# Performance work log

Hardware: AMD Instinct MI355X
Metric: run time of the kernel (lower is better)

The kernel has to match this reference:

```python
import jax, jax.numpy as jnp
import numpy as np

EPS = 1e-5  # torch BatchNorm1d default eps


def _bn(x, g, b, m, v):
    # x: [B, C, L]; params: [C] (inference-mode BN using running stats)
    scale = g / jnp.sqrt(v + EPS)
    return x * scale[None, :, None] + (b - m * scale)[None, :, None]


def setup_inputs() -> dict:
    key = jax.random.key(0)
    ks = jax.random.split(key, 16)
    B, C, L, I = 32, 256, 4096, 64
    d = {
        "x_a": jax.random.normal(ks[0], (B, C, L), jnp.float32),
        "x_b": jax.random.normal(ks[1], (B, C, L), jnp.float32),
        "x_c": jax.random.normal(ks[2], (B, C, L), jnp.float32),
        "w1": jax.random.normal(ks[3], (4, I, C), jnp.float32) * 0.05,
        "b1": jax.random.normal(ks[4], (4, I), jnp.float32) * 0.05,
        "bn1_g": jax.random.uniform(ks[5], (4, I), jnp.float32, 0.5, 1.5),
        "bn1_b": jax.random.normal(ks[6], (4, I), jnp.float32) * 0.05,
        "bn1_m": jax.random.normal(ks[7], (4, I), jnp.float32) * 0.05,
        "bn1_v": jax.random.uniform(ks[8], (4, I), jnp.float32, 0.5, 1.5),
        "w2": jax.random.normal(ks[9], (4, C, I), jnp.float32) * 0.05,
        "b2": jax.random.normal(ks[10], (4, C), jnp.float32) * 0.05,
        "bn2_g": jax.random.uniform(ks[11], (4, C), jnp.float32, 0.5, 1.5),
        "bn2_b": jax.random.normal(ks[12], (4, C), jnp.float32) * 0.05,
        "bn2_m": jax.random.normal(ks[13], (4, C), jnp.float32) * 0.05,
        "bn2_v": jax.random.uniform(ks[14], (4, C), jnp.float32, 0.5, 1.5),
    }
    return d


def reference(x_a, x_b, x_c, w1, b1, bn1_g, bn1_b, bn1_m, bn1_v,
              w2, b2, bn2_g, bn2_b, bn2_m, bn2_v):
    def att(x, i, global_pool):
        # branch i: conv1x1 -> BN -> ReLU -> conv1x1 -> BN
        h = jnp.mean(x, axis=-1, keepdims=True) if global_pool else x
        h = jnp.einsum('bcl,ic->bil', h, w1[i]) + b1[i][None, :, None]
        h = jax.nn.relu(_bn(h, bn1_g[i], bn1_b[i], bn1_m[i], bn1_v[i]))
        h = jnp.einsum('bil,ci->bcl', h, w2[i]) + b2[i][None, :, None]
        return _bn(h, bn2_g[i], bn2_b[i], bn2_m[i], bn2_v[i])

    x_ab = x_a + x_b
    wei = jax.nn.sigmoid(att(x_ab, 0, False) + att(x_ab, 1, True))  # [B,C,L]
    xo1 = x_a * wei + x_b * (1.0 - wei)

    x_abc = xo1 + x_c
    wei2 = jax.nn.sigmoid(att(x_abc, 2, False) + att(x_abc, 3, True))
    # NOTE: faithful to source: second blend uses (1 - wei), not (1 - wei2)
    xo2 = xo1 * wei2 + x_c * (1.0 - wei)
    return (xo1 + xo2) * 0.5
```

## Files before the change

### kernel.cpp

```cpp
#include <hip/hip_runtime.h>
#include <cstddef>

#define EPS_ 1e-5f


#define OFF_W1T0 0
#define OFF_W2T0 16384
#define OFF_W1T2 32768
#define OFF_W2T2 49152
#define OFF_C1_0 65536
#define OFF_C2_0 65600
#define OFF_C1_2 65856
#define OFF_C2_2 65920
#define OFF_MEANAB 66176
#define OFF_SUMABC 74368
#define OFF_G1 82560
#define OFF_G3 90752
#define OFF_XO1 131072
#define OFF_P 33685504

__global__ __launch_bounds__(256) void k_prep(
    const float* __restrict__ w1, const float* __restrict__ b1,
    const float* __restrict__ bn1g, const float* __restrict__ bn1b,
    const float* __restrict__ bn1m, const float* __restrict__ bn1v,
    const float* __restrict__ w2, const float* __restrict__ b2,
    const float* __restrict__ bn2g, const float* __restrict__ bn2b,
    const float* __restrict__ bn2m, const float* __restrict__ bn2v,
    float* __restrict__ ws)
{
  int idx = blockIdx.x * 256 + threadIdx.x;
  if (idx < 32768) {
    int slot = idx >> 14, r = idx & 16383;
    int br = slot << 1;
    int c = r >> 6, i = r & 63;
    int gi = (br << 6) + i;
    float s1 = bn1g[gi] / sqrtf(bn1v[gi] + EPS_);
    ws[OFF_W1T0 + (slot << 15) + r] = w1[gi * 256 + c] * s1;
  } else if (idx < 65536) {
    int j = idx - 32768;
    int slot = j >> 14, r = j & 16383;
    int br = slot << 1;
    int i = r >> 8, c = r & 255;
    int gc = (br << 8) + c;
    float s2 = bn2g[gc] / sqrtf(bn2v[gc] + EPS_);
    ws[OFF_W2T0 + (slot << 15) + r] = w2[gc * 64 + i] * s2;
  } else if (idx < 65664) {
    int j = idx - 65536;
    int slot = j >> 6, i = j & 63;
    int gi = ((slot << 1) << 6) + i;
    float s1 = bn1g[gi] / sqrtf(bn1v[gi] + EPS_);
    ws[OFF_C1_0 + slot * 320 + i] = bn1b[gi] + s1 * (b1[gi] - bn1m[gi]);
  } else if (idx < 66176) {
    int j = idx - 65664;
    int slot = j >> 8, c = j & 255;
    int gc = ((slot << 1) << 8) + c;
    float s2 = bn2g[gc] / sqrtf(bn2v[gc] + EPS_);
    ws[OFF_C2_0 + slot * 320 + c] = bn2b[gc] + s2 * (b2[gc] - bn2m[gc]);
  } else if (idx < 74368) {
    ws[OFF_SUMABC + (idx - 66176)] = 0.0f;
  }
}

__global__ __launch_bounds__(256) void k_mean_ab(
    const float* __restrict__ xa, const float* __restrict__ xb,
    float* __restrict__ mean_ab)
{
  const int row = blockIdx.x;
  const size_t base4 = (size_t)row * 1024;
  const float4* a4 = (const float4*)xa;
  const float4* b4 = (const float4*)xb;
  float s = 0.0f;
#pragma unroll
  for (int k = 0; k < 4; ++k) {
    float4 va = a4[base4 + k * 256 + threadIdx.x];
    float4 vb = b4[base4 + k * 256 + threadIdx.x];
    s += (va.x + vb.x) + (va.y + vb.y) + (va.z + vb.z) + (va.w + vb.w);
  }
#pragma unroll
  for (int m = 32; m; m >>= 1) s += __shfl_xor(s, m, 64);
  __shared__ float part[4];
  if ((threadIdx.x & 63) == 0) part[threadIdx.x >> 6] = s;
  __syncthreads();
  if (threadIdx.x == 0)
    mean_ab[row] = (part[0] + part[1] + part[2] + part[3]) * (1.0f / 4096.0f);
}

__global__ __launch_bounds__(256) void k_gatt(
    int br, const float* __restrict__ vin, float scale,
    const float* __restrict__ w1, const float* __restrict__ b1,
    const float* __restrict__ bn1g, const float* __restrict__ bn1b,
    const float* __restrict__ bn1m, const float* __restrict__ bn1v,
    const float* __restrict__ w2, const float* __restrict__ b2,
    const float* __restrict__ bn2g, const float* __restrict__ bn2b,
    const float* __restrict__ bn2m, const float* __restrict__ bn2v,
    float* __restrict__ gout)
{
  const int b = blockIdx.x, tid = threadIdx.x;
  __shared__ float xs[256];
  __shared__ float as[64];
  xs[tid] = vin[(b << 8) + tid] * scale;
  __syncthreads();
  if (tid < 64) {
    const int gi = (br << 6) + tid;
    const float* wr = w1 + gi * 256;
    float acc = 0.0f;
#pragma unroll 8
    for (int c = 0; c < 256; ++c) acc = fmaf(wr[c], xs[c], acc);
    float s1 = bn1g[gi] / sqrtf(bn1v[gi] + EPS_);
    float h = s1 * (acc + b1[gi] - bn1m[gi]) + bn1b[gi];
    as[tid] = fmaxf(h, 0.0f);
  }
  __syncthreads();
  const int gc = (br << 8) + tid;
  const float* wr2 = w2 + gc * 64;
  float acc = 0.0f;
#pragma unroll 8
  for (int i = 0; i < 64; ++i) acc = fmaf(wr2[i], as[i], acc);
  float s2 = bn2g[gc] / sqrtf(bn2v[gc] + EPS_);
  gout[(b << 8) + tid] = s2 * (acc + b2[gc] - bn2m[gc]) + bn2b[gc];
}

__global__ __launch_bounds__(512, 6) void k_local1(
    const float* __restrict__ xa, const float* __restrict__ xb,
    const float* __restrict__ xc,
    const float* __restrict__ W1t, const float* __restrict__ W2t,
    const float* __restrict__ c1, const float* __restrict__ c2,
    const float* __restrict__ g1,
    float* __restrict__ xo1, float* __restrict__ pbuf,
    float* __restrict__ sumabc)
{
  const int tid = threadIdx.x;
  const int lane = tid & 63;
  const int wav = __builtin_amdgcn_readfirstlane(tid >> 6);
  const int b = blockIdx.x >> 6;
  const int l0 = (blockIdx.x & 63) << 6;
  __shared__ float xs[2][64][64];
  __shared__ float hs[64][64];
  __shared__ float cgs[256];
  const size_t rowbase = ((size_t)b << 20) + (size_t)l0;

  if (tid < 256) cgs[tid] = c2[tid] + g1[(b << 8) + tid];

  const int srow = tid >> 4;
  const int scol = (tid & 15) << 2;

  float4 ra0, rb0, ra1, rb1;
  {
    const size_t o0 = rowbase + ((size_t)srow << 12) + scol;
    const size_t o1 = rowbase + ((size_t)(srow + 32) << 12) + scol;
    ra0 = *(const float4*)(xa + o0); rb0 = *(const float4*)(xb + o0);
    ra1 = *(const float4*)(xa + o1); rb1 = *(const float4*)(xb + o1);
  }
  {
    float4 v0 = {ra0.x + rb0.x, ra0.y + rb0.y, ra0.z + rb0.z, ra0.w + rb0.w};
    float4 v1 = {ra1.x + rb1.x, ra1.y + rb1.y, ra1.z + rb1.z, ra1.w + rb1.w};
    *(float4*)&xs[0][srow][scol] = v0;
    *(float4*)&xs[0][srow + 32][scol] = v1;
  }
  __syncthreads();

  const int i0 = wav << 3;
  float acc[8] = {0.f, 0.f, 0.f, 0.f, 0.f, 0.f, 0.f, 0.f};
  const float* __restrict__ w1base = W1t + i0;
  for (int kb = 0; kb < 4; ++kb) {
    if (kb < 3) {
      const size_t cb = rowbase + ((size_t)((kb + 1) << 6) << 12);
      const size_t o0 = cb + ((size_t)srow << 12) + scol;
      const size_t o1 = cb + ((size_t)(srow + 32) << 12) + scol;
      ra0 = *(const float4*)(xa + o0); rb0 = *(const float4*)(xb + o0);
      ra1 = *(const float4*)(xa + o1); rb1 = *(const float4*)(xb + o1);
    }
    const float* __restrict__ wr0 = w1base + ((kb << 6) << 6);
    const int pb = kb & 1;
#pragma unroll 2
    for (int c = 0; c < 64; ++c) {
      const float xv = xs[pb][c][lane];
      const float* wr = wr0 + (c << 6);
#pragma unroll
      for (int i = 0; i < 8; ++i) acc[i] = fmaf(wr[i], xv, acc[i]);
    }
    __syncthreads();
    if (kb < 3) {
      const int nb = (kb + 1) & 1;
      float4 v0 = {ra0.x + rb0.x, ra0.y + rb0.y, ra0.z + rb0.z, ra0.w + rb0.w};
      float4 v1 = {ra1.x + rb1.x, ra1.y + rb1.y, ra1.z + rb1.z, ra1.w + rb1.w};
      *(float4*)&xs[nb][srow][scol] = v0;
      *(float4*)&xs[nb][srow + 32][scol] = v1;
      __syncthreads();
    }
  }

#pragma unroll
  for (int i = 0; i < 8; ++i)
    hs[i0 + i][lane] = fmaxf(acc[i] + c1[i0 + i], 0.0f);
  __syncthreads();

  const int cc0 = wav << 5;
  float acc2[32];
#pragma unroll
  for (int j = 0; j < 32; ++j) acc2[j] = 0.0f;
  const float* __restrict__ w2base = W2t + cc0;
  for (int ii = 0; ii < 64; ++ii) {
    const float hv = hs[ii][lane];
    const float* wr = w2base + (ii << 8);
#pragma unroll
    for (int j = 0; j < 32; ++j) acc2[j] = fmaf(wr[j], hv, acc2[j]);
  }

  for (int j = 0; j < 32; ++j) {
    const int cc = cc0 + j;
    const size_t off = rowbase + ((size_t)cc << 12) + (size_t)lane;
    const float w = 1.0f / (1.0f + __expf(-(acc2[j] + cgs[cc])));
    const float a = xa[off], bb = xb[off], q = xc[off];
    const float xo = fmaf(a - bb, w, bb);
    xo1[off] = xo;
    pbuf[off] = 0.5f * (1.0f - w) * q;
    float s = xo + q;
#pragma unroll
    for (int m = 1; m < 64; m <<= 1) s += __shfl_xor(s, m, 64);
    if (lane == 0) atomicAdd(&sumabc[(b << 8) + cc], s);
  }
}

__global__ __launch_bounds__(512, 6) void k_local2(
    const float* __restrict__ xo1, const float* __restrict__ xc,
    const float* __restrict__ pbuf,
    const float* __restrict__ W1t, const float* __restrict__ W2t,
    const float* __restrict__ c1, const float* __restrict__ c2,
    const float* __restrict__ g3,
    float* __restrict__ outp)
{
  const int tid = threadIdx.x;
  const int lane = tid & 63;
  const int wav = __builtin_amdgcn_readfirstlane(tid >> 6);
  const int b = blockIdx.x >> 6;
  const int l0 = (blockIdx.x & 63) << 6;
  __shared__ float xs[2][64][64];
  __shared__ float hs[64][64];
  __shared__ float cgs[256];
  const size_t rowbase = ((size_t)b << 20) + (size_t)l0;

  if (tid < 256) cgs[tid] = c2[tid] + g3[(b << 8) + tid];

  const int srow = tid >> 4;
  const int scol = (tid & 15) << 2;

  float4 ra0, rb0, ra1, rb1;
  {
    const size_t o0 = rowbase + ((size_t)srow << 12) + scol;
    const size_t o1 = rowbase + ((size_t)(srow + 32) << 12) + scol;
    ra0 = *(const float4*)(xo1 + o0); rb0 = *(const float4*)(xc + o0);
    ra1 = *(const float4*)(xo1 + o1); rb1 = *(const float4*)(xc + o1);
  }
  {
    float4 v0 = {ra0.x + rb0.x, ra0.y + rb0.y, ra0.z + rb0.z, ra0.w + rb0.w};
    float4 v1 = {ra1.x + rb1.x, ra1.y + rb1.y, ra1.z + rb1.z, ra1.w + rb1.w};
    *(float4*)&xs[0][srow][scol] = v0;
    *(float4*)&xs[0][srow + 32][scol] = v1;
  }
  __syncthreads();

  const int i0 = wav << 3;
  float acc[8] = {0.f, 0.f, 0.f, 0.f, 0.f, 0.f, 0.f, 0.f};
  const float* __restrict__ w1base = W1t + i0;
  for (int kb = 0; kb < 4; ++kb) {
    if (kb < 3) {
      const size_t cb = rowbase + ((size_t)((kb + 1) << 6) << 12);
      const size_t o0 = cb + ((size_t)srow << 12) + scol;
      const size_t o1 = cb + ((size_t)(srow + 32) << 12) + scol;
      ra0 = *(const float4*)(xo1 + o0); rb0 = *(const float4*)(xc + o0);
      ra1 = *(const float4*)(xo1 + o1); rb1 = *(const float4*)(xc + o1);
    }
    const float* __restrict__ wr0 = w1base + ((kb << 6) << 6);
    const int pb = kb & 1;
#pragma unroll 2
    for (int c = 0; c < 64; ++c) {
      const float xv = xs[pb][c][lane];
      const float* wr = wr0 + (c << 6);
#pragma unroll
      for (int i = 0; i < 8; ++i) acc[i] = fmaf(wr[i], xv, acc[i]);
    }
    __syncthreads();
    if (kb < 3) {
      const int nb = (kb + 1) & 1;
      float4 v0 = {ra0.x + rb0.x, ra0.y + rb0.y, ra0.z + rb0.z, ra0.w + rb0.w};
      float4 v1 = {ra1.x + rb1.x, ra1.y + rb1.y, ra1.z + rb1.z, ra1.w + rb1.w};
      *(float4*)&xs[nb][srow][scol] = v0;
      *(float4*)&xs[nb][srow + 32][scol] = v1;
      __syncthreads();
    }
  }

#pragma unroll
  for (int i = 0; i < 8; ++i)
    hs[i0 + i][lane] = fmaxf(acc[i] + c1[i0 + i], 0.0f);
  __syncthreads();

  const int cc0 = wav << 5;
  float acc2[32];
#pragma unroll
  for (int j = 0; j < 32; ++j) acc2[j] = 0.0f;
  const float* __restrict__ w2base = W2t + cc0;
  for (int ii = 0; ii < 64; ++ii) {
    const float hv = hs[ii][lane];
    const float* wr = w2base + (ii << 8);
#pragma unroll
    for (int j = 0; j < 32; ++j) acc2[j] = fmaf(wr[j], hv, acc2[j]);
  }

  for (int j = 0; j < 32; ++j) {
    const int cc = cc0 + j;
    const size_t off = rowbase + ((size_t)cc << 12) + (size_t)lane;
    const float w2s = 1.0f / (1.0f + __expf(-(acc2[j] + cgs[cc])));
    const float xov = xo1[off];
    const float pv = pbuf[off];
    outp[off] = fmaf(0.5f * xov, w2s, fmaf(0.5f, xov, pv));
  }
}

extern "C" void kernel_launch(void* const* d_in, const int* in_sizes, int n_in,
                              void* d_out, int out_size, void* d_ws, size_t ws_size,
                              hipStream_t stream) {
  const float* xa = (const float*)d_in[0];
  const float* xb = (const float*)d_in[1];
  const float* xc = (const float*)d_in[2];
  const float* w1 = (const float*)d_in[3];
  const float* b1 = (const float*)d_in[4];
  const float* bn1g = (const float*)d_in[5];
  const float* bn1b = (const float*)d_in[6];
  const float* bn1m = (const float*)d_in[7];
  const float* bn1v = (const float*)d_in[8];
  const float* w2 = (const float*)d_in[9];
  const float* b2 = (const float*)d_in[10];
  const float* bn2g = (const float*)d_in[11];
  const float* bn2b = (const float*)d_in[12];
  const float* bn2m = (const float*)d_in[13];
  const float* bn2v = (const float*)d_in[14];
  float* ws = (float*)d_ws;
  float* outp = (float*)d_out;

  float* W1t0 = ws + OFF_W1T0;
  float* W2t0 = ws + OFF_W2T0;
  float* W1t2 = ws + OFF_W1T2;
  float* W2t2 = ws + OFF_W2T2;
  float* c1_0 = ws + OFF_C1_0;
  float* c2_0 = ws + OFF_C2_0;
  float* c1_2 = ws + OFF_C1_2;
  float* c2_2 = ws + OFF_C2_2;
  float* mean_ab = ws + OFF_MEANAB;
  float* sum_abc = ws + OFF_SUMABC;
  float* g1 = ws + OFF_G1;
  float* g3 = ws + OFF_G3;
  float* xo1 = ws + OFF_XO1;
  float* pbuf = ws + OFF_P;

  k_prep<<<291, 256, 0, stream>>>(w1, b1, bn1g, bn1b, bn1m, bn1v,
                                  w2, b2, bn2g, bn2b, bn2m, bn2v, ws);
  k_mean_ab<<<8192, 256, 0, stream>>>(xa, xb, mean_ab);
  k_gatt<<<32, 256, 0, stream>>>(1, mean_ab, 1.0f,
                                 w1, b1, bn1g, bn1b, bn1m, bn1v,
                                 w2, b2, bn2g, bn2b, bn2m, bn2v, g1);
  k_local1<<<2048, 512, 0, stream>>>(xa, xb, xc, W1t0, W2t0, c1_0, c2_0, g1,
                                     xo1, pbuf, sum_abc);
  k_gatt<<<32, 256, 0, stream>>>(3, sum_abc, 1.0f / 4096.0f,
                                 w1, b1, bn1g, bn1b, bn1m, bn1v,
                                 w2, b2, bn2g, bn2b, bn2m, bn2v, g3);
  k_local2<<<2048, 512, 0, stream>>>(xo1, xc, pbuf, W1t2, W2t2, c1_2, c2_2, g3,
                                     outp);
}
```

Measured before the change: 911.3 us.

## Use fp16 MFMA for conv1x1 branches and store sigmoid weights in half

Replaces the scalar-FMA 1x1 conv GEMMs in both local kernels with 16x16x32 fp16 MFMA instructions. Weights are pre-swizzled into MFMA operand layout in k_prep, and activations are loaded straight from global memory into registers with no LDS staging. The fp32 pbuf intermediate is replaced by an fp16 copy of the first sigmoid weight, which cuts write and read traffic between kernels. The mean of x_c is computed in the first reduction pass so local1 no longer reads x_c. The trade-off is fp16 precision on activations and weights, plus strided per-element global loads of the activations.

```diff
diff --git a/kernel.cpp b/kernel.cpp
--- a/kernel.cpp
+++ b/kernel.cpp
@@ -1,23 +1,26 @@
 #include <hip/hip_runtime.h>
 #include <cstddef>
+#include <cstdint>
 
 #define EPS_ 1e-5f
 
 
-#define OFF_W1T0 0
-#define OFF_W2T0 16384
-#define OFF_W1T2 32768
-#define OFF_W2T2 49152
-#define OFF_C1_0 65536
-#define OFF_C2_0 65600
-#define OFF_C1_2 65856
-#define OFF_C2_2 65920
-#define OFF_MEANAB 66176
-#define OFF_SUMABC 74368
-#define OFF_G1 82560
-#define OFF_G3 90752
+typedef _Float16 f16x8 __attribute__((ext_vector_type(8)));
+typedef float   f32x4 __attribute__((ext_vector_type(4)));
+
+#define OFF_C1_0 32768
+#define OFF_C1_2 32832
+#define OFF_C2_0 32896
+#define OFF_C2_2 33152
+#define OFF_MEANAB 33408
+#define OFF_MEANC  41600
+#define OFF_SUMXO  49792
+#define OFF_G1 57984
+#define OFF_G3 66176
 #define OFF_XO1 131072
-#define OFF_P 33685504
+#define OFF_WEI16 33685504
+
+#define MFMA16(A, B, C) __builtin_amdgcn_mfma_f32_16x16x32_f16((A), (B), (C), 0, 0, 0)
 
 __global__ __launch_bounds__(256) void k_prep(
     const float* __restrict__ w1, const float* __restrict__ b1,
@@ -28,65 +31,82 @@
     const float* __restrict__ bn2m, const float* __restrict__ bn2v,
     float* __restrict__ ws)
 {
+  _Float16* ws16 = (_Float16*)ws;
   int idx = blockIdx.x * 256 + threadIdx.x;
   if (idx < 32768) {
     int slot = idx >> 14, r = idx & 16383;
+    int it = r >> 12, kk = (r >> 9) & 7, lane = (r >> 3) & 63, e = r & 7;
     int br = slot << 1;
-    int c = r >> 6, i = r & 63;
+    int i = it * 16 + (lane & 15);
+    int c = kk * 32 + ((lane >> 4) << 2) + (e & 3) + ((e >> 2) << 4);
     int gi = (br << 6) + i;
     float s1 = bn1g[gi] / sqrtf(bn1v[gi] + EPS_);
-    ws[OFF_W1T0 + (slot << 15) + r] = w1[gi * 256 + c] * s1;
+    ws16[slot * 16384 + r] = (_Float16)(w1[gi * 256 + c] * s1);
   } else if (idx < 65536) {
-    int j = idx - 32768;
-    int slot = j >> 14, r = j & 16383;
+    int d = idx - 32768;
+    int slot = d >> 14, r = d & 16383;
+    int rt = r >> 10, kk2 = (r >> 9) & 1, lane = (r >> 3) & 63, e = r & 7;
     int br = slot << 1;
-    int i = r >> 8, c = r & 255;
-    int gc = (br << 8) + c;
+    int crow = rt * 16 + (lane & 15);
+    int ik = kk2 * 32 + ((lane >> 4) << 2) + (e & 3) + ((e >> 2) << 4);
+    int gc = (br << 8) + crow;
     float s2 = bn2g[gc] / sqrtf(bn2v[gc] + EPS_);
-    ws[OFF_W2T0 + (slot << 15) + r] = w2[gc * 64 + i] * s2;
+    ws16[32768 + slot * 16384 + r] = (_Float16)(w2[gc * 64 + ik] * s2);
   } else if (idx < 65664) {
-    int j = idx - 65536;
-    int slot = j >> 6, i = j & 63;
-    int gi = ((slot << 1) << 6) + i;
+    int d = idx - 65536;
+    int slot = d >> 6, i = d & 63;
+    int gi = slot * 128 + i;
     float s1 = bn1g[gi] / sqrtf(bn1v[gi] + EPS_);
-    ws[OFF_C1_0 + slot * 320 + i] = bn1b[gi] + s1 * (b1[gi] - bn1m[gi]);
+    ws[OFF_C1_0 + slot * 64 + i] = bn1b[gi] + s1 * (b1[gi] - bn1m[gi]);
   } else if (idx < 66176) {
-    int j = idx - 65664;
-    int slot = j >> 8, c = j & 255;
-    int gc = ((slot << 1) << 8) + c;
+    int d = idx - 65664;
+    int slot = d >> 8, cc = d & 255;
+    int gc = slot * 512 + cc;
     float s2 = bn2g[gc] / sqrtf(bn2v[gc] + EPS_);
-    ws[OFF_C2_0 + slot * 320 + c] = bn2b[gc] + s2 * (b2[gc] - bn2m[gc]);
+    ws[OFF_C2_0 + slot * 256 + cc] = bn2b[gc] + s2 * (b2[gc] - bn2m[gc]);
   } else if (idx < 74368) {
-    ws[OFF_SUMABC + (idx - 66176)] = 0.0f;
-  }
-}
-
-__global__ __launch_bounds__(256) void k_mean_ab(
+    ws[OFF_SUMXO + (idx - 66176)] = 0.0f;
+  }
+}
+
+__global__ __launch_bounds__(256) void k_mean3(
     const float* __restrict__ xa, const float* __restrict__ xb,
-    float* __restrict__ mean_ab)
+    const float* __restrict__ xc,
+    float* __restrict__ mean_ab, float* __restrict__ mean_c)
 {
   const int row = blockIdx.x;
   const size_t base4 = (size_t)row * 1024;
   const float4* a4 = (const float4*)xa;
   const float4* b4 = (const float4*)xb;
-  float s = 0.0f;
+  const float4* c4 = (const float4*)xc;
+  float sab = 0.0f, sc = 0.0f;
 #pragma unroll
   for (int k = 0; k < 4; ++k) {
     float4 va = a4[base4 + k * 256 + threadIdx.x];
     float4 vb = b4[base4 + k * 256 + threadIdx.x];
-    s += (va.x + vb.x) + (va.y + vb.y) + (va.z + vb.z) + (va.w + vb.w);
-  }
-#pragma unroll
-  for (int m = 32; m; m >>= 1) s += __shfl_xor(s, m, 64);
-  __shared__ float part[4];
-  if ((threadIdx.x & 63) == 0) part[threadIdx.x >> 6] = s;
-  __syncthreads();
-  if (threadIdx.x == 0)
-    mean_ab[row] = (part[0] + part[1] + part[2] + part[3]) * (1.0f / 4096.0f);
+    float4 vc = c4[base4 + k * 256 + threadIdx.x];
+    sab += (va.x + vb.x) + (va.y + vb.y) + (va.z + vb.z) + (va.w + vb.w);
+    sc += vc.x + vc.y + vc.z + vc.w;
+  }
+#pragma unroll
+  for (int m = 32; m; m >>= 1) {
+    sab += __shfl_xor(sab, m, 64);
+    sc += __shfl_xor(sc, m, 64);
+  }
+  __shared__ float pab[4], pc[4];
+  if ((threadIdx.x & 63) == 0) {
+    pab[threadIdx.x >> 6] = sab; pc[threadIdx.x >> 6] = sc;
+  }
+  __syncthreads();
+  if (threadIdx.x == 0) {
+    mean_ab[row] = (pab[0] + pab[1] + pab[2] + pab[3]) * (1.0f / 4096.0f);
+    mean_c[row] = (pc[0] + pc[1] + pc[2] + pc[3]) * (1.0f / 4096.0f);
+  }
 }
 
 __global__ __launch_bounds__(256) void k_gatt(
-    int br, const float* __restrict__ vin, float scale,
+    int br, const float* __restrict__ vinA, float scaleA,
+    const float* __restrict__ vinB, float scaleB,
     const float* __restrict__ w1, const float* __restrict__ b1,
     const float* __restrict__ bn1g, const float* __restrict__ bn1b,
     const float* __restrict__ bn1m, const float* __restrict__ bn1v,
@@ -98,7 +118,7 @@
   const int b = blockIdx.x, tid = threadIdx.x;
   __shared__ float xs[256];
   __shared__ float as[64];
-  xs[tid] = vin[(b << 8) + tid] * scale;
+  xs[tid] = vinA[(b << 8) + tid] * scaleA + vinB[(b << 8) + tid] * scaleB;
   __syncthreads();
   if (tid < 64) {
     const int gi = (br << 6) + tid;
@@ -120,201 +140,167 @@
   gout[(b << 8) + tid] = s2 * (acc + b2[gc] - bn2m[gc]) + bn2b[gc];
 }
 
-__global__ __launch_bounds__(512, 6) void k_local1(
+__global__ __launch_bounds__(256) void k_local1(
     const float* __restrict__ xa, const float* __restrict__ xb,
-    const float* __restrict__ xc,
-    const float* __restrict__ W1t, const float* __restrict__ W2t,
+    const _Float16* __restrict__ W1A, const _Float16* __restrict__ W2A,
     const float* __restrict__ c1, const float* __restrict__ c2,
     const float* __restrict__ g1,
-    float* __restrict__ xo1, float* __restrict__ pbuf,
-    float* __restrict__ sumabc)
+    float* __restrict__ xo1, _Float16* __restrict__ wei16,
+    float* __restrict__ sumxo)
 {
   const int tid = threadIdx.x;
   const int lane = tid & 63;
-  const int wav = __builtin_amdgcn_readfirstlane(tid >> 6);
+  const int ct = tid >> 6;
   const int b = blockIdx.x >> 6;
   const int l0 = (blockIdx.x & 63) << 6;
-  __shared__ float xs[2][64][64];
-  __shared__ float hs[64][64];
   __shared__ float cgs[256];
-  const size_t rowbase = ((size_t)b << 20) + (size_t)l0;
-
-  if (tid < 256) cgs[tid] = c2[tid] + g1[(b << 8) + tid];
-
-  const int srow = tid >> 4;
-  const int scol = (tid & 15) << 2;
-
-  float4 ra0, rb0, ra1, rb1;
-  {
-    const size_t o0 = rowbase + ((size_t)srow << 12) + scol;
-    const size_t o1 = rowbase + ((size_t)(srow + 32) << 12) + scol;
-    ra0 = *(const float4*)(xa + o0); rb0 = *(const float4*)(xb + o0);
-    ra1 = *(const float4*)(xa + o1); rb1 = *(const float4*)(xb + o1);
-  }
-  {
-    float4 v0 = {ra0.x + rb0.x, ra0.y + rb0.y, ra0.z + rb0.z, ra0.w + rb0.w};
-    float4 v1 = {ra1.x + rb1.x, ra1.y + rb1.y, ra1.z + rb1.z, ra1.w + rb1.w};
-    *(float4*)&xs[0][srow][scol] = v0;
-    *(float4*)&xs[0][srow + 32][scol] = v1;
-  }
-  __syncthreads();
-
-  const int i0 = wav << 3;
-  float acc[8] = {0.f, 0.f, 0.f, 0.f, 0.f, 0.f, 0.f, 0.f};
-  const float* __restrict__ w1base = W1t + i0;
-  for (int kb = 0; kb < 4; ++kb) {
-    if (kb < 3) {
-      const size_t cb = rowbase + ((size_t)((kb + 1) << 6) << 12);
-      const size_t o0 = cb + ((size_t)srow << 12) + scol;
-      const size_t o1 = cb + ((size_t)(srow + 32) << 12) + scol;
-      ra0 = *(const float4*)(xa + o0); rb0 = *(const float4*)(xb + o0);
-      ra1 = *(const float4*)(xa + o1); rb1 = *(const float4*)(xb + o1);
-    }
-    const float* __restrict__ wr0 = w1base + ((kb << 6) << 6);
-    const int pb = kb & 1;
+  __shared__ float c1s[64];
+  __shared__ float sblk[256];
+
+  cgs[tid] = c2[tid] + g1[(b << 8) + tid];
+  if (tid < 64) c1s[tid] = c1[tid];
+  sblk[tid] = 0.0f;
+  __syncthreads();
+
+  const int g4 = (lane >> 4) << 2;
+  const int col = l0 + (ct << 4) + (lane & 15);
+  const size_t gbase = ((size_t)b << 20) + (size_t)col;
+  const float* __restrict__ xab = xa + gbase;
+  const float* __restrict__ xbb = xb + gbase;
+
+  f32x4 acc1[4] = {{0,0,0,0},{0,0,0,0},{0,0,0,0},{0,0,0,0}};
+  const f16x8* __restrict__ w1a = (const f16x8*)W1A;
+#pragma unroll
+  for (int kk = 0; kk < 8; ++kk) {
+    union { f16x8 v; _Float16 e[8]; } bu;
+#pragma unroll
+    for (int e = 0; e < 8; ++e) {
+      const int c = (kk << 5) + g4 + (e & 3) + ((e >> 2) << 4);
+      const size_t o = (size_t)c << 12;
+      bu.e[e] = (_Float16)(xab[o] + xbb[o]);
+    }
+    acc1[0] = MFMA16(w1a[(0 * 8 + kk) * 64 + lane], bu.v, acc1[0]);
+    acc1[1] = MFMA16(w1a[(1 * 8 + kk) * 64 + lane], bu.v, acc1[1]);
+    acc1[2] = MFMA16(w1a[(2 * 8 + kk) * 64 + lane], bu.v, acc1[2]);
+    acc1[3] = MFMA16(w1a[(3 * 8 + kk) * 64 + lane], bu.v, acc1[3]);
+  }
+
+  f16x8 hb[2];
+#pragma unroll
+  for (int half = 0; half < 2; ++half) {
+    union { f16x8 v; _Float16 e[8]; } hu;
+#pragma unroll
+    for (int q = 0; q < 2; ++q) {
+      const int it = half * 2 + q;
+      const int ib = it * 16 + g4;
+#pragma unroll
+      for (int r = 0; r < 4; ++r)
+        hu.e[q * 4 + r] = (_Float16)fmaxf(acc1[it][r] + c1s[ib + r], 0.0f);
+    }
+    hb[half] = hu.v;
+  }
+
+  const f16x8* __restrict__ w2a = (const f16x8*)W2A;
 #pragma unroll 2
-    for (int c = 0; c < 64; ++c) {
-      const float xv = xs[pb][c][lane];
-      const float* wr = wr0 + (c << 6);
-#pragma unroll
-      for (int i = 0; i < 8; ++i) acc[i] = fmaf(wr[i], xv, acc[i]);
-    }
-    __syncthreads();
-    if (kb < 3) {
-      const int nb = (kb + 1) & 1;
-      float4 v0 = {ra0.x + rb0.x, ra0.y + rb0.y, ra0.z + rb0.z, ra0.w + rb0.w};
-      float4 v1 = {ra1.x + rb1.x, ra1.y + rb1.y, ra1.z + rb1.z, ra1.w + rb1.w};
-      *(float4*)&xs[nb][srow][scol] = v0;
-      *(float4*)&xs[nb][srow + 32][scol] = v1;
-      __syncthreads();
-    }
-  }
-
-#pragma unroll
-  for (int i = 0; i < 8; ++i)
-    hs[i0 + i][lane] = fmaxf(acc[i] + c1[i0 + i], 0.0f);
-  __syncthreads();
-
-  const int cc0 = wav << 5;
-  float acc2[32];
-#pragma unroll
-  for (int j = 0; j < 32; ++j) acc2[j] = 0.0f;
-  const float* __restrict__ w2base = W2t + cc0;
-  for (int ii = 0; ii < 64; ++ii) {
-    const float hv = hs[ii][lane];
-    const float* wr = w2base + (ii << 8);
-#pragma unroll
-    for (int j = 0; j < 32; ++j) acc2[j] = fmaf(wr[j], hv, acc2[j]);
-  }
-
-  for (int j = 0; j < 32; ++j) {
-    const int cc = cc0 + j;
-    const size_t off = rowbase + ((size_t)cc << 12) + (size_t)lane;
-    const float w = 1.0f / (1.0f + __expf(-(acc2[j] + cgs[cc])));
-    const float a = xa[off], bb = xb[off], q = xc[off];
-    const float xo = fmaf(a - bb, w, bb);
-    xo1[off] = xo;
-    pbuf[off] = 0.5f * (1.0f - w) * q;
-    float s = xo + q;
-#pragma unroll
-    for (int m = 1; m < 64; m <<= 1) s += __shfl_xor(s, m, 64);
-    if (lane == 0) atomicAdd(&sumabc[(b << 8) + cc], s);
-  }
-}
-
-__global__ __launch_bounds__(512, 6) void k_local2(
-    const float* __restrict__ xo1, const float* __restrict__ xc,
-    const float* __restrict__ pbuf,
-    const float* __restrict__ W1t, const float* __restrict__ W2t,
+  for (int rt = 0; rt < 16; ++rt) {
+    f32x4 acc2 = {0, 0, 0, 0};
+    acc2 = MFMA16(w2a[(rt * 2 + 0) * 64 + lane], hb[0], acc2);
+    acc2 = MFMA16(w2a[(rt * 2 + 1) * 64 + lane], hb[1], acc2);
+#pragma unroll
+    for (int r = 0; r < 4; ++r) {
+      const int c = (rt << 4) + g4 + r;
+      const size_t o = (size_t)c << 12;
+      const float t = acc2[r] + cgs[c];
+      const float w = 1.0f / (1.0f + __expf(-t));
+      const float av = xab[o], bv = xbb[o];
+      const float xo = fmaf(av - bv, w, bv);
+      xo1[gbase + o] = xo;
+      wei16[gbase + o] = (_Float16)w;
+      float s = xo;
+      s += __shfl_xor(s, 1, 64); s += __shfl_xor(s, 2, 64);
+      s += __shfl_xor(s, 4, 64); s += __shfl_xor(s, 8, 64);
+      if ((lane & 15) == 0) atomicAdd(&sblk[c], s);
+    }
+  }
+  __syncthreads();
+  atomicAdd(&sumxo[(b << 8) + tid], sblk[tid]);
+}
+
+__global__ __launch_bounds__(256) void k_local2(
+    const float* __restrict__ xo1g, const float* __restrict__ xc,
+    const _Float16* __restrict__ W1A, const _Float16* __restrict__ W2A,
     const float* __restrict__ c1, const float* __restrict__ c2,
-    const float* __restrict__ g3,
+    const float* __restrict__ g3, const _Float16* __restrict__ wei16,
     float* __restrict__ outp)
 {
   const int tid = threadIdx.x;
   const int lane = tid & 63;
-  const int wav = __builtin_amdgcn_readfirstlane(tid >> 6);
+  const int ct = tid >> 6;
   const int b = blockIdx.x >> 6;
   const int l0 = (blockIdx.x & 63) << 6;
-  __shared__ float xs[2][64][64];
-  __shared__ float hs[64][64];
   __shared__ float cgs[256];
-  const size_t rowbase = ((size_t)b << 20) + (size_t)l0;
-
-  if (tid < 256) cgs[tid] = c2[tid] + g3[(b << 8) + tid];
-
-  const int srow = tid >> 4;
-  const int scol = (tid & 15) << 2;
-
-  float4 ra0, rb0, ra1, rb1;
-  {
-    const size_t o0 = rowbase + ((size_t)srow << 12) + scol;
-    const size_t o1 = rowbase + ((size_t)(srow + 32) << 12) + scol;
-    ra0 = *(const float4*)(xo1 + o0); rb0 = *(const float4*)(xc + o0);
-    ra1 = *(const float4*)(xo1 + o1); rb1 = *(const float4*)(xc + o1);
-  }
-  {
-    float4 v0 = {ra0.x + rb0.x, ra0.y + rb0.y, ra0.z + rb0.z, ra0.w + rb0.w};
-    float4 v1 = {ra1.x + rb1.x, ra1.y + rb1.y, ra1.z + rb1.z, ra1.w + rb1.w};
-    *(float4*)&xs[0][srow][scol] = v0;
-    *(float4*)&xs[0][srow + 32][scol] = v1;
-  }
-  __syncthreads();
-
-  const int i0 = wav << 3;
-  float acc[8] = {0.f, 0.f, 0.f, 0.f, 0.f, 0.f, 0.f, 0.f};
-  const float* __restrict__ w1base = W1t + i0;
-  for (int kb = 0; kb < 4; ++kb) {
-    if (kb < 3) {
-      const size_t cb = rowbase + ((size_t)((kb + 1) << 6) << 12);
-      const size_t o0 = cb + ((size_t)srow << 12) + scol;
-      const size_t o1 = cb + ((size_t)(srow + 32) << 12) + scol;
-      ra0 = *(const float4*)(xo1 + o0); rb0 = *(const float4*)(xc + o0);
-      ra1 = *(const float4*)(xo1 + o1); rb1 = *(const float4*)(xc + o1);
-    }
-    const float* __restrict__ wr0 = w1base + ((kb << 6) << 6);
-    const int pb = kb & 1;
+  __shared__ float c1s[64];
+
+  cgs[tid] = c2[tid] + g3[(b << 8) + tid];
+  if (tid < 64) c1s[tid] = c1[tid];
+  __syncthreads();
+
+  const int g4 = (lane >> 4) << 2;
+  const int col = l0 + (ct << 4) + (lane & 15);
+  const size_t gbase = ((size_t)b << 20) + (size_t)col;
+  const float* __restrict__ xob = xo1g + gbase;
+  const float* __restrict__ xcb = xc + gbase;
+
+  f32x4 acc1[4] = {{0,0,0,0},{0,0,0,0},{0,0,0,0},{0,0,0,0}};
+  const f16x8* __restrict__ w1a = (const f16x8*)W1A;
+#pragma unroll
+  for (int kk = 0; kk < 8; ++kk) {
+    union { f16x8 v; _Float16 e[8]; } bu;
+#pragma unroll
+    for (int e = 0; e < 8; ++e) {
+      const int c = (kk << 5) + g4 + (e & 3) + ((e >> 2) << 4);
+      const size_t o = (size_t)c << 12;
+      bu.e[e] = (_Float16)(xob[o] + xcb[o]);
+    }
+    acc1[0] = MFMA16(w1a[(0 * 8 + kk) * 64 + lane], bu.v, acc1[0]);
+    acc1[1] = MFMA16(w1a[(1 * 8 + kk) * 64 + lane], bu.v, acc1[1]);
+    acc1[2] = MFMA16(w1a[(2 * 8 + kk) * 64 + lane], bu.v, acc1[2]);
+    acc1[3] = MFMA16(w1a[(3 * 8 + kk) * 64 + lane], bu.v, acc1[3]);
+  }
+
+  f16x8 hb[2];
+#pragma unroll
+  for (int half = 0; half < 2; ++half) {
+    union { f16x8 v; _Float16 e[8]; } hu;
+#pragma unroll
+    for (int q = 0; q < 2; ++q) {
+      const int it = half * 2 + q;
+      const int ib = it * 16 + g4;
+#pragma unroll
+      for (int r = 0; r < 4; ++r)
+        hu.e[q * 4 + r] = (_Float16)fmaxf(acc1[it][r] + c1s[ib + r], 0.0f);
+    }
+    hb[half] = hu.v;
+  }
+
+  const f16x8* __restrict__ w2a = (const f16x8*)W2A;
 #pragma unroll 2
-    for (int c = 0; c < 64; ++c) {
-      const float xv = xs[pb][c][lane];
-      const float* wr = wr0 + (c << 6);
-#pragma unroll
-      for (int i = 0; i < 8; ++i) acc[i] = fmaf(wr[i], xv, acc[i]);
-    }
-    __syncthreads();
-    if (kb < 3) {
-      const int nb = (kb + 1) & 1;
-      float4 v0 = {ra0.x + rb0.x, ra0.y + rb0.y, ra0.z + rb0.z, ra0.w + rb0.w};
-      float4 v1 = {ra1.x + rb1.x, ra1.y + rb1.y, ra1.z + rb1.z, ra1.w + rb1.w};
-      *(float4*)&xs[nb][srow][scol] = v0;
-      *(float4*)&xs[nb][srow + 32][scol] = v1;
-      __syncthreads();
-    }
-  }
-
-#pragma unroll
-  for (int i = 0; i < 8; ++i)
-    hs[i0 + i][lane] = fmaxf(acc[i] + c1[i0 + i], 0.0f);
-  __syncthreads();
-
-  const int cc0 = wav << 5;
-  float acc2[32];
-#pragma unroll
-  for (int j = 0; j < 32; ++j) acc2[j] = 0.0f;
-  const float* __restrict__ w2base = W2t + cc0;
-  for (int ii = 0; ii < 64; ++ii) {
-    const float hv = hs[ii][lane];
-    const float* wr = w2base + (ii << 8);
-#pragma unroll
-    for (int j = 0; j < 32; ++j) acc2[j] = fmaf(wr[j], hv, acc2[j]);
-  }
-
-  for (int j = 0; j < 32; ++j) {
-    const int cc = cc0 + j;
-    const size_t off = rowbase + ((size_t)cc << 12) + (size_t)lane;
-    const float w2s = 1.0f / (1.0f + __expf(-(acc2[j] + cgs[cc])));
-    const float xov = xo1[off];
-    const float pv = pbuf[off];
-    outp[off] = fmaf(0.5f * xov, w2s, fmaf(0.5f, xov, pv));
+  for (int rt = 0; rt < 16; ++rt) {
+    f32x4 acc2 = {0, 0, 0, 0};
+    acc2 = MFMA16(w2a[(rt * 2 + 0) * 64 + lane], hb[0], acc2);
+    acc2 = MFMA16(w2a[(rt * 2 + 1) * 64 + lane], hb[1], acc2);
+#pragma unroll
+    for (int r = 0; r < 4; ++r) {
+      const int c = (rt << 4) + g4 + r;
+      const size_t o = (size_t)c << 12;
+      const float t = acc2[r] + cgs[c];
+      const float w2v = 1.0f / (1.0f + __expf(-t));
+      const float xov = xob[o];
+      const float xcv = xcb[o];
+      const float w1v = (float)wei16[gbase + o];
+      outp[gbase + o] = fmaf(0.5f * xov, w2v,
+                             fmaf(0.5f, xov, 0.5f * (1.0f - w1v) * xcv));
+    }
   }
 }
 
@@ -337,34 +323,36 @@
   const float* bn2m = (const float*)d_in[13];
   const float* bn2v = (const float*)d_in[14];
   float* ws = (float*)d_ws;
+  _Float16* ws16 = (_Float16*)d_ws;
   float* outp = (float*)d_out;
 
-  float* W1t0 = ws + OFF_W1T0;
-  float* W2t0 = ws + OFF_W2T0;
-  float* W1t2 = ws + OFF_W1T2;
-  float* W2t2 = ws + OFF_W2T2;
+  _Float16* W1A0 = ws16;
+  _Float16* W1A2 = ws16 + 16384;
+  _Float16* W2A0 = ws16 + 32768;
+  _Float16* W2A2 = ws16 + 49152;
   float* c1_0 = ws + OFF_C1_0;
+  float* c1_2 = ws + OFF_C1_2;
   float* c2_0 = ws + OFF_C2_0;
-  float* c1_2 = ws + OFF_C1_2;
   float* c2_2 = ws + OFF_C2_2;
   float* mean_ab = ws + OFF_MEANAB;
-  float* sum_abc = ws + OFF_SUMABC;
+  float* mean_c = ws + OFF_MEANC;
+  float* sumxo = ws + OFF_SUMXO;
   float* g1 = ws + OFF_G1;
   float* g3 = ws + OFF_G3;
   float* xo1 = ws + OFF_XO1;
-  float* pbuf = ws + OFF_P;
+  _Float16* wei16 = (_Float16*)(ws + OFF_WEI16);
 
   k_prep<<<291, 256, 0, stream>>>(w1, b1, bn1g, bn1b, bn1m, bn1v,
                                   w2, b2, bn2g, bn2b, bn2m, bn2v, ws);
-  k_mean_ab<<<8192, 256, 0, stream>>>(xa, xb, mean_ab);
-  k_gatt<<<32, 256, 0, stream>>>(1, mean_ab, 1.0f,
+  k_mean3<<<8192, 256, 0, stream>>>(xa, xb, xc, mean_ab, mean_c);
+  k_gatt<<<32, 256, 0, stream>>>(1, mean_ab, 1.0f, mean_ab, 0.0f,
                                  w1, b1, bn1g, bn1b, bn1m, bn1v,
                                  w2, b2, bn2g, bn2b, bn2m, bn2v, g1);
-  k_local1<<<2048, 512, 0, stream>>>(xa, xb, xc, W1t0, W2t0, c1_0, c2_0, g1,
-                                     xo1, pbuf, sum_abc);
-  k_gatt<<<32, 256, 0, stream>>>(3, sum_abc, 1.0f / 4096.0f,
+  k_local1<<<2048, 256, 0, stream>>>(xa, xb, W1A0, W2A0, c1_0, c2_0, g1,
+                                     xo1, wei16, sumxo);
+  k_gatt<<<32, 256, 0, stream>>>(3, sumxo, 1.0f / 4096.0f, mean_c, 1.0f,
                                  w1, b1, bn1g, bn1b, bn1m, bn1v,
                                  w2, b2, bn2g, bn2b, bn2m, bn2v, g3);
-  k_local2<<<2048, 512, 0, stream>>>(xo1, xc, pbuf, W1t2, W2t2, c1_2, c2_2, g3,
-                                     outp);
-}
+  k_local2<<<2048, 256, 0, stream>>>(xo1, xc, W1A2, W2A2, c1_2, c2_2, g3,
+                                     wei16, outp);
+}
```

Measured after the change: 749.3 us. -17.8%, faster.
